# Optimization experiments

Hardware: AMD Instinct MI355X
Metric: run time of the kernel (lower is better)

The kernel has to match this reference:

```python
import jax, jax.numpy as jnp
import numpy as np

KQ = 512
NEG = -1e9


def setup_inputs() -> dict:
    key = jax.random.key(0)
    k1, k2, k3, k4, k5 = jax.random.split(key, 5)
    B, NQ, NK, D, V, O = 16, 1024, 2048, 512, 512, 256
    return {
        "keys": jax.random.normal(k1, (B, NK, D), dtype=jnp.float32),
        "queries": jax.random.normal(k2, (B, NQ, D), dtype=jnp.float32),
        "values": jax.random.normal(k3, (B, NK, V), dtype=jnp.float32),
        "mask": jax.random.randint(k4, (B, NQ, NK), 0, 2, dtype=jnp.int32),
        "W_resize": jax.random.normal(k5, (O, V), dtype=jnp.float32) * (1.0 / np.sqrt(V)),
        "b_resize": jnp.zeros((O,), dtype=jnp.float32),
    }


def reference(keys, queries, values, mask, W_resize, b_resize):
    # score: scaled dot product  [B, NQ, NK]
    logits = jnp.einsum("bqd,bkd->bqk", queries, keys) / jnp.sqrt(jnp.float32(KQ))
    logits = jnp.where(mask == 0, jnp.float32(NEG), logits)
    attn = jax.nn.softmax(logits, axis=-1)
    # context: [B, NQ, V]
    context = jnp.einsum("bqk,bkv->bqv", attn, values)
    # resize to out_size
    context = jnp.einsum("bqv,ov->bqo", context, W_resize) + b_resize
    return context
```

## Files before the change

kernel.cpp:

```cpp
#include <hip/hip_runtime.h>

#define BB   16
#define NQ   1024
#define NK   2048
#define DD   512
#define VV   512
#define OO   256
#define SCALE 0.044194173824159216f

typedef __attribute__((ext_vector_type(4))) float f32x4;
typedef __attribute__((ext_vector_type(8))) short s16x8;

#define AS1(p) ((const __attribute__((address_space(1))) void*)(p))
#define AS3(p) ((__attribute__((address_space(3))) void*)(p))

__device__ __forceinline__ unsigned short f2bf(float f) {
  unsigned u = __float_as_uint(f);
  u += 0x7fffu + ((u >> 16) & 1u);
  return (unsigned short)(u >> 16);
}
__device__ __forceinline__ float bf2f(unsigned short b) {
  return __uint_as_float(((unsigned)b) << 16);
}

__device__ __forceinline__ void gemm_bt_core(
    const unsigned short* __restrict__ Abase,
    const unsigned short* __restrict__ Bbase,
    int K,
    unsigned short* As, unsigned short* Bs,
    f32x4 acc[4][4])
{
  const int t = threadIdx.x;
  const int w = t >> 6;
  const int l = t & 63;
  const int srow = l >> 2;
  const int scol = (l & 3) * 8;
  const int r0 = (w * 2 + 0) * 16 + srow;
  const int r1 = (w * 2 + 1) * 16 + srow;
  const int lds0 = (w * 2 + 0) * 512 + l * 8;
  const int lds1 = (w * 2 + 1) * 512 + l * 8;
  const int wm = (w >> 1) * 64;
  const int wn = (w & 1) * 64;
  const int lm = l & 15;
  const int lq = l >> 4;

  for (int kt = 0; kt < K; kt += 32) {
    __builtin_amdgcn_global_load_lds(AS1(Abase + (size_t)r0 * K + kt + scol), AS3(As + lds0), 16, 0, 0);
    __builtin_amdgcn_global_load_lds(AS1(Abase + (size_t)r1 * K + kt + scol), AS3(As + lds1), 16, 0, 0);
    __builtin_amdgcn_global_load_lds(AS1(Bbase + (size_t)r0 * K + kt + scol), AS3(Bs + lds0), 16, 0, 0);
    __builtin_amdgcn_global_load_lds(AS1(Bbase + (size_t)r1 * K + kt + scol), AS3(Bs + lds1), 16, 0, 0);
    __syncthreads();
    s16x8 af[4], bfr[4];
    #pragma unroll
    for (int i = 0; i < 4; ++i) {
      af[i]  = *(const s16x8*)(As + (wm + i * 16 + lm) * 32 + lq * 8);
      bfr[i] = *(const s16x8*)(Bs + (wn + i * 16 + lm) * 32 + lq * 8);
    }
    #pragma unroll
    for (int mi = 0; mi < 4; ++mi)
      #pragma unroll
      for (int ni = 0; ni < 4; ++ni)
        acc[mi][ni] = __builtin_amdgcn_mfma_f32_16x16x32_bf16(af[mi], bfr[ni], acc[mi][ni], 0, 0, 0);
    __syncthreads();
  }
}


#define CS_STRIDE 136

__global__ __launch_bounds__(256)
void qk_kernel(const unsigned short* __restrict__ Qb,
               const unsigned short* __restrict__ Kb,
               const int* __restrict__ mask,
               unsigned short* __restrict__ S,
               float* __restrict__ sums)
{
  const int b  = blockIdx.z;
  const int tm = blockIdx.y;
  const int tn = blockIdx.x;
  __shared__ unsigned short smem[128 * CS_STRIDE];
  unsigned short* As = smem;
  unsigned short* Bs = smem + 4096;
  unsigned short* Cs = smem;
  const int t = threadIdx.x, w = t >> 6, l = t & 63;
  const int trow = t >> 4, tcol = (t & 15) * 8;

  unsigned mbits0 = 0, mbits1 = 0;
  #pragma unroll
  for (int it = 0; it < 8; ++it) {
    const int row = it * 16 + trow;
    const size_t gbase = ((size_t)b * NQ + tm * 128 + row) * NK + tn * 128 + tcol;
    const int4 m0 = *(const int4*)(mask + gbase);
    const int4 m1 = *(const int4*)(mask + gbase + 4);
    unsigned byte = (m0.x ? 1u : 0u) | (m0.y ? 2u : 0u) | (m0.z ? 4u : 0u) | (m0.w ? 8u : 0u)
                  | (m1.x ? 16u : 0u) | (m1.y ? 32u : 0u) | (m1.z ? 64u : 0u) | (m1.w ? 128u : 0u);
    if (it < 4) mbits0 |= byte << (8 * it);
    else        mbits1 |= byte << (8 * (it - 4));
  }

  f32x4 acc[4][4];
  #pragma unroll
  for (int i = 0; i < 4; ++i)
    #pragma unroll
    for (int j = 0; j < 4; ++j) acc[i][j] = (f32x4){0.f, 0.f, 0.f, 0.f};

  gemm_bt_core(Qb + ((size_t)b * NQ + tm * 128) * DD,
               Kb + ((size_t)b * NK + tn * 128) * DD, DD, As, Bs, acc);

  const int wm = (w >> 1) * 64, wn = (w & 1) * 64;
  const int lm = l & 15, lq = l >> 4;
  #pragma unroll
  for (int mi = 0; mi < 4; ++mi)
    #pragma unroll
    for (int ni = 0; ni < 4; ++ni)
      #pragma unroll
      for (int r = 0; r < 4; ++r)
        Cs[(wm + mi * 16 + lq * 4 + r) * CS_STRIDE + wn + ni * 16 + lm] =
            f2bf(acc[mi][ni][r] * SCALE);
  __syncthreads();

  #pragma unroll
  for (int it = 0; it < 8; ++it) {
    const int row = it * 16 + trow;
    const int gq = tm * 128 + row;
    const size_t gbase = ((size_t)b * NQ + gq) * NK + tn * 128 + tcol;
    s16x8 v = *(const s16x8*)(Cs + row * CS_STRIDE + tcol);
    const unsigned byte = ((it < 4) ? (mbits0 >> (8 * it)) : (mbits1 >> (8 * (it - 4)))) & 0xffu;
    float e[8];
    #pragma unroll
    for (int j = 0; j < 8; ++j)
      e[j] = (byte >> j & 1u) ? __expf(bf2f((unsigned short)v[j])) : 0.f;
    float sp = 0.f;
    #pragma unroll
    for (int j = 0; j < 8; ++j) sp += e[j];
    #pragma unroll
    for (int off = 8; off > 0; off >>= 1) sp += __shfl_down(sp, off, 16);
    if ((t & 15) == 0) atomicAdd(&sums[(size_t)b * NQ + gq], sp);
    s16x8 o;
    #pragma unroll
    for (int j = 0; j < 8; ++j) o[j] = (short)f2bf(e[j]);
    *(s16x8*)(S + gbase) = o;
  }
}

__global__ __launch_bounds__(256)
void pv_kernel(const unsigned short* __restrict__ P,
               const unsigned short* __restrict__ Vt,
               const float* __restrict__ sums,
               unsigned short* __restrict__ Ctx)
{
  const int b  = blockIdx.z;
  const int tm = blockIdx.y;
  const int tn = blockIdx.x;
  __shared__ unsigned short smem[128 * CS_STRIDE];
  __shared__ float Ls[128];
  unsigned short* As = smem;
  unsigned short* Bs = smem + 4096;
  unsigned short* Cs = smem;
  const int t = threadIdx.x;
  if (t < 128) Ls[t] = 1.0f / sums[(size_t)b * NQ + tm * 128 + t];
  f32x4 acc[4][4];
  #pragma unroll
  for (int i = 0; i < 4; ++i)
    #pragma unroll
    for (int j = 0; j < 4; ++j) acc[i][j] = (f32x4){0.f, 0.f, 0.f, 0.f};

  gemm_bt_core(P  + ((size_t)b * NQ + tm * 128) * NK,
               Vt + ((size_t)b * VV + tn * 128) * NK, NK, As, Bs, acc);

  const int w = t >> 6, l = t & 63;
  const int wm = (w >> 1) * 64, wn = (w & 1) * 64;
  const int lm = l & 15, lq = l >> 4;
  #pragma unroll
  for (int mi = 0; mi < 4; ++mi)
    #pragma unroll
    for (int ni = 0; ni < 4; ++ni)
      #pragma unroll
      for (int r = 0; r < 4; ++r) {
        const int row = wm + mi * 16 + lq * 4 + r;
        Cs[row * CS_STRIDE + wn + ni * 16 + lm] = f2bf(acc[mi][ni][r] * Ls[row]);
      }
  __syncthreads();
  const int trow = t >> 4, tcol = (t & 15) * 8;
  #pragma unroll
  for (int it = 0; it < 8; ++it) {
    const int row = it * 16 + trow;
    s16x8 v = *(const s16x8*)(Cs + row * CS_STRIDE + tcol);
    *(s16x8*)(Ctx + ((size_t)b * NQ + tm * 128 + row) * VV + tn * 128 + tcol) = v;
  }
}

#define CSF_STRIDE 136
__global__ __launch_bounds__(256)
void rs_kernel(const unsigned short* __restrict__ Ctx,
               const unsigned short* __restrict__ Wb,
               const float* __restrict__ bias,
               float* __restrict__ out)
{
  const int tm = blockIdx.y;
  const int tn = blockIdx.x;
  __shared__ float smemf[128 * CSF_STRIDE];
  unsigned short* As = (unsigned short*)smemf;
  unsigned short* Bs = (unsigned short*)smemf + 4096;
  float* Cs = smemf;
  f32x4 acc[4][4];
  #pragma unroll
  for (int i = 0; i < 4; ++i)
    #pragma unroll
    for (int j = 0; j < 4; ++j) acc[i][j] = (f32x4){0.f, 0.f, 0.f, 0.f};

  gemm_bt_core(Ctx + (size_t)tm * 128 * VV,
               Wb + (size_t)tn * 128 * VV, VV, As, Bs, acc);

  const int t = threadIdx.x, w = t >> 6, l = t & 63;
  const int wm = (w >> 1) * 64, wn = (w & 1) * 64;
  const int lm = l & 15, lq = l >> 4;
  #pragma unroll
  for (int mi = 0; mi < 4; ++mi)
    #pragma unroll
    for (int ni = 0; ni < 4; ++ni)
      #pragma unroll
      for (int r = 0; r < 4; ++r)
        Cs[(wm + mi * 16 + lq * 4 + r) * CSF_STRIDE + wn + ni * 16 + lm] = acc[mi][ni][r];
  __syncthreads();
  const int trow = t >> 4, tcol = (t & 15) * 8;
  #pragma unroll
  for (int it = 0; it < 8; ++it) {
    const int row = it * 16 + trow;
    f32x4 a = *(const f32x4*)(Cs + row * CSF_STRIDE + tcol);
    f32x4 c = *(const f32x4*)(Cs + row * CSF_STRIDE + tcol + 4);
    const int gn = tn * 128 + tcol;
    const f32x4 b0 = *(const f32x4*)(bias + gn);
    const f32x4 b1 = *(const f32x4*)(bias + gn + 4);
    a += b0; c += b1;
    float* o = out + (size_t)(tm * 128 + row) * OO + gn;
    *(f32x4*)o = a;
    *(f32x4*)(o + 4) = c;
  }
}

#define VT_STRIDE 68
__device__ __forceinline__ void cvt8(const float* __restrict__ in,
                                     unsigned short* __restrict__ out, int i)
{
  const float4* p = (const float4*)in + (size_t)i * 2;
  const float4 a = p[0], b = p[1];
  s16x8 o;
  o[0] = (short)f2bf(a.x); o[1] = (short)f2bf(a.y);
  o[2] = (short)f2bf(a.z); o[3] = (short)f2bf(a.w);
  o[4] = (short)f2bf(b.x); o[5] = (short)f2bf(b.y);
  o[6] = (short)f2bf(b.z); o[7] = (short)f2bf(b.w);
  ((s16x8*)out)[i] = o;
}

__global__ __launch_bounds__(256)
void prep_kernel(const float* __restrict__ q, const float* __restrict__ k,
                 const float* __restrict__ w, const float* __restrict__ v,
                 unsigned short* __restrict__ Qb, unsigned short* __restrict__ Kb,
                 unsigned short* __restrict__ Wb, unsigned short* __restrict__ Vt,
                 float* __restrict__ sums)
{
  __shared__ float tile[64 * VT_STRIDE];
  const int bid = blockIdx.x;
  const int t = threadIdx.x;
  if (bid < 4096) {
    cvt8(q, Qb, bid * 256 + t);
  } else if (bid < 12288) {
    cvt8(k, Kb, (bid - 4096) * 256 + t);
  } else if (bid < 12352) {
    cvt8(w, Wb, (bid - 12288) * 256 + t);
  } else if (bid < 16448) {
    const int flat = bid - 12352;
    const int b  = flat >> 8;
    const int rem = flat & 255;
    const int k0 = (rem >> 3) * 64;
    const int v0 = (rem & 7) * 64;
    const int lr = t >> 4, lc4 = (t & 15) * 4;
    #pragma unroll
    for (int j = 0; j < 4; ++j) {
      const int row = lr + j * 16;
      const float4 x = *(const float4*)(v + ((size_t)b * NK + k0 + row) * VV + v0 + lc4);
      *(float4*)(tile + row * VT_STRIDE + lc4) = x;
    }
    __syncthreads();
    const int vr = t >> 3, kx = (t & 7) * 8;
    #pragma unroll
    for (int j = 0; j < 2; ++j) {
      const int vv = vr + j * 32;
      s16x8 o;
      #pragma unroll
      for (int i = 0; i < 8; ++i) o[i] = (short)f2bf(tile[(kx + i) * VT_STRIDE + vv]);
      *(s16x8*)(Vt + ((size_t)b * VV + v0 + vv) * NK + k0 + kx) = o;
    }
  } else {
    const int i = (bid - 16448) * 256 + t;
    if (i < BB * NQ) sums[i] = 0.f;
  }
}

extern "C" void kernel_launch(void* const* d_in, const int* in_sizes, int n_in,
                              void* d_out, int out_size, void* d_ws, size_t ws_size,
                              hipStream_t stream)
{
  const float* keys    = (const float*)d_in[0];
  const float* queries = (const float*)d_in[1];
  const float* values  = (const float*)d_in[2];
  const int*   mask    = (const int*)  d_in[3];
  const float* W       = (const float*)d_in[4];
  const float* bias    = (const float*)d_in[5];
  float* out = (float*)d_out;

  char* ws = (char*)d_ws;
  unsigned short* Qb = (unsigned short*)(ws);
  unsigned short* Kb = (unsigned short*)(ws + (16ull << 20));
  unsigned short* Vt = (unsigned short*)(ws + (48ull << 20));
  unsigned short* Wb = (unsigned short*)(ws + (80ull << 20));
  unsigned short* S  = (unsigned short*)(ws + (81ull << 20));
  float* sums        = (float*)(ws + (145ull << 20));
  unsigned short* Ctx = Qb;

  prep_kernel<<<dim3(16512), 256, 0, stream>>>(queries, keys, W, values,
                                               Qb, Kb, Wb, Vt, sums);
  qk_kernel<<<dim3(NK / 128, NQ / 128, BB), 256, 0, stream>>>(Qb, Kb, mask, S, sums);
  pv_kernel<<<dim3(VV / 128, NQ / 128, BB), 256, 0, stream>>>(S, Vt, sums, Ctx);
  rs_kernel<<<dim3(OO / 128, (BB * NQ) / 128, 1), 256, 0, stream>>>(Ctx, Wb, bias, out);
}
```

Measured before the change: 465.0 us.

## Fuse QK, masked softmax and PV into a single flash-style kernel

Replaces the separate QK-score kernel (which wrote the bf16 probability matrix to global memory) and the PV kernel with one fused kernel. Each block handles 32 query rows and loops over 128-key tiles, computing scores, masked exponentials and row sums in shared memory, then accumulating P·V in registers. This removes the 64MB intermediate score write and reread and the atomic sum buffer. In exchange the tiles are smaller (32 rows), each block rereads K and V for every 32 queries, and there are many __syncthreads per tile. Like the old code, it skips max-subtraction in the softmax, relying on small logits.

```diff
diff --git a/kernel.cpp b/kernel.cpp
--- a/kernel.cpp
+++ b/kernel.cpp
@@ -21,6 +21,176 @@
 }
 __device__ __forceinline__ float bf2f(unsigned short b) {
   return __uint_as_float(((unsigned)b) << 16);
+}
+
+#define MFMA16(a, b, c) __builtin_amdgcn_mfma_f32_16x16x32_bf16(a, b, c, 0, 0, 0)
+
+__global__ __launch_bounds__(256)
+void flash_kernel(const unsigned short* __restrict__ Qb,
+                  const unsigned short* __restrict__ Kb,
+                  const unsigned short* __restrict__ Vt,
+                  const int* __restrict__ mask,
+                  unsigned short* __restrict__ Ctx)
+{
+  const int b  = blockIdx.y;
+  const int q0 = blockIdx.x * 32;
+  __shared__ unsigned short Qs[32 * 520];
+  __shared__ unsigned short KVs[16640];
+  __shared__ unsigned short Ps[32 * 136];
+  __shared__ float rowsum[32];
+  __shared__ float invs[32];
+
+  const int t = threadIdx.x, w = t >> 6, l = t & 63;
+  const int lm = l & 15, lq = l >> 4;
+  const int sr = l >> 2, sc = (l & 3) * 8;
+
+  f32x4 oacc[2][8];
+  #pragma unroll
+  for (int mi = 0; mi < 2; ++mi)
+    #pragma unroll
+    for (int ni = 0; ni < 8; ++ni) oacc[mi][ni] = (f32x4){0.f, 0.f, 0.f, 0.f};
+
+  #pragma unroll
+  for (int i = 0; i < 8; ++i) {
+    const int row = w * 8 + i;
+    __builtin_amdgcn_global_load_lds(
+        AS1(Qb + ((size_t)(b * NQ + q0 + row)) * DD + l * 8),
+        AS3(Qs + row * 520 + l * 8), 16, 0, 0);
+  }
+  if (t < 32) rowsum[t] = 0.f;
+
+  const int prow = t >> 3, pcol = (t & 7) * 16;
+
+  #pragma unroll 1
+  for (int kt = 0; kt < 16; ++kt) {
+    const size_t mbase = ((size_t)(b * NQ + q0 + prow)) * NK + kt * 128 + pcol;
+    const int4 pm0 = *(const int4*)(mask + mbase);
+    const int4 pm1 = *(const int4*)(mask + mbase + 4);
+    const int4 pm2 = *(const int4*)(mask + mbase + 8);
+    const int4 pm3 = *(const int4*)(mask + mbase + 12);
+
+    f32x4 sacc[2][2];
+    #pragma unroll
+    for (int mi = 0; mi < 2; ++mi)
+      #pragma unroll
+      for (int ni = 0; ni < 2; ++ni) sacc[mi][ni] = (f32x4){0.f, 0.f, 0.f, 0.f};
+
+    const unsigned short* Kbase = Kb + ((size_t)(b * NK + kt * 128)) * DD;
+    #pragma unroll
+    for (int rnd = 0; rnd < 8; ++rnd) {
+      __syncthreads();
+      #pragma unroll
+      for (int c = 0; c < 2; ++c)
+        #pragma unroll
+        for (int i = 0; i < 2; ++i)
+          __builtin_amdgcn_global_load_lds(
+              AS1(Kbase + (size_t)(w * 32 + i * 16 + sr) * DD + rnd * 64 + c * 32 + sc),
+              AS3(KVs + c * 4096 + (w * 32 + i * 16) * 32 + l * 8), 16, 0, 0);
+      __syncthreads();
+      #pragma unroll
+      for (int c = 0; c < 2; ++c) {
+        s16x8 qf[2], kf[2];
+        #pragma unroll
+        for (int mi = 0; mi < 2; ++mi)
+          qf[mi] = *(const s16x8*)(Qs + (mi * 16 + lm) * 520 + rnd * 64 + c * 32 + lq * 8);
+        #pragma unroll
+        for (int ni = 0; ni < 2; ++ni)
+          kf[ni] = *(const s16x8*)(KVs + c * 4096 + (w * 32 + ni * 16 + lm) * 32 + lq * 8);
+        #pragma unroll
+        for (int mi = 0; mi < 2; ++mi)
+          #pragma unroll
+          for (int ni = 0; ni < 2; ++ni)
+            sacc[mi][ni] = MFMA16(qf[mi], kf[ni], sacc[mi][ni]);
+      }
+    }
+
+    #pragma unroll
+    for (int mi = 0; mi < 2; ++mi)
+      #pragma unroll
+      for (int ni = 0; ni < 2; ++ni)
+        #pragma unroll
+        for (int r = 0; r < 4; ++r)
+          Ps[(mi * 16 + lq * 4 + r) * 136 + w * 32 + ni * 16 + lm] =
+              f2bf(sacc[mi][ni][r] * SCALE);
+    __syncthreads();
+
+    {
+      s16x8 p0 = *(const s16x8*)(Ps + prow * 136 + pcol);
+      s16x8 p1 = *(const s16x8*)(Ps + prow * 136 + pcol + 8);
+      float e[16];
+      e[0]  = pm0.x ? __expf(bf2f((unsigned short)p0[0])) : 0.f;
+      e[1]  = pm0.y ? __expf(bf2f((unsigned short)p0[1])) : 0.f;
+      e[2]  = pm0.z ? __expf(bf2f((unsigned short)p0[2])) : 0.f;
+      e[3]  = pm0.w ? __expf(bf2f((unsigned short)p0[3])) : 0.f;
+      e[4]  = pm1.x ? __expf(bf2f((unsigned short)p0[4])) : 0.f;
+      e[5]  = pm1.y ? __expf(bf2f((unsigned short)p0[5])) : 0.f;
+      e[6]  = pm1.z ? __expf(bf2f((unsigned short)p0[6])) : 0.f;
+      e[7]  = pm1.w ? __expf(bf2f((unsigned short)p0[7])) : 0.f;
+      e[8]  = pm2.x ? __expf(bf2f((unsigned short)p1[0])) : 0.f;
+      e[9]  = pm2.y ? __expf(bf2f((unsigned short)p1[1])) : 0.f;
+      e[10] = pm2.z ? __expf(bf2f((unsigned short)p1[2])) : 0.f;
+      e[11] = pm2.w ? __expf(bf2f((unsigned short)p1[3])) : 0.f;
+      e[12] = pm3.x ? __expf(bf2f((unsigned short)p1[4])) : 0.f;
+      e[13] = pm3.y ? __expf(bf2f((unsigned short)p1[5])) : 0.f;
+      e[14] = pm3.z ? __expf(bf2f((unsigned short)p1[6])) : 0.f;
+      e[15] = pm3.w ? __expf(bf2f((unsigned short)p1[7])) : 0.f;
+      float sp = 0.f;
+      s16x8 o0, o1;
+      #pragma unroll
+      for (int j = 0; j < 8; ++j) { o0[j] = (short)f2bf(e[j]); sp += e[j]; }
+      #pragma unroll
+      for (int j = 0; j < 8; ++j) { o1[j] = (short)f2bf(e[8 + j]); sp += e[8 + j]; }
+      *(s16x8*)(Ps + prow * 136 + pcol) = o0;
+      *(s16x8*)(Ps + prow * 136 + pcol + 8) = o1;
+      #pragma unroll
+      for (int off = 4; off > 0; off >>= 1) sp += __shfl_down(sp, off, 8);
+      if ((t & 7) == 0) rowsum[prow] += sp;
+    }
+
+    #pragma unroll
+    for (int cs = 0; cs < 4; ++cs) {
+      __syncthreads();
+      #pragma unroll
+      for (int i = 0; i < 8; ++i)
+        __builtin_amdgcn_global_load_lds(
+            AS1(Vt + ((size_t)(b * VV + w * 128 + i * 16 + sr)) * NK + kt * 128 + cs * 32 + sc),
+            AS3(KVs + (w * 128 + i * 16) * 32 + l * 8), 16, 0, 0);
+      __syncthreads();
+      s16x8 pf[2], vf[8];
+      #pragma unroll
+      for (int mi = 0; mi < 2; ++mi)
+        pf[mi] = *(const s16x8*)(Ps + (mi * 16 + lm) * 136 + cs * 32 + lq * 8);
+      #pragma unroll
+      for (int ni = 0; ni < 8; ++ni)
+        vf[ni] = *(const s16x8*)(KVs + (w * 128 + ni * 16 + lm) * 32 + lq * 8);
+      #pragma unroll
+      for (int mi = 0; mi < 2; ++mi)
+        #pragma unroll
+        for (int ni = 0; ni < 8; ++ni)
+          oacc[mi][ni] = MFMA16(pf[mi], vf[ni], oacc[mi][ni]);
+    }
+  }
+
+  __syncthreads();
+  if (t < 32) invs[t] = 1.f / rowsum[t];
+  __syncthreads();
+  #pragma unroll
+  for (int mi = 0; mi < 2; ++mi)
+    #pragma unroll
+    for (int ni = 0; ni < 8; ++ni)
+      #pragma unroll
+      for (int r = 0; r < 4; ++r) {
+        const int row = mi * 16 + lq * 4 + r;
+        KVs[row * 520 + w * 128 + ni * 16 + lm] = f2bf(oacc[mi][ni][r] * invs[row]);
+      }
+  __syncthreads();
+  const int orow = t >> 3;
+  #pragma unroll
+  for (int it = 0; it < 8; ++it) {
+    const int col = (t & 7) * 8 + it * 64;
+    s16x8 v = *(const s16x8*)(KVs + orow * 520 + col);
+    *(s16x8*)(Ctx + ((size_t)(b * NQ + q0 + orow)) * VV + col) = v;
+  }
 }
 
 __device__ __forceinline__ void gemm_bt_core(
@@ -60,133 +230,8 @@
     for (int mi = 0; mi < 4; ++mi)
       #pragma unroll
       for (int ni = 0; ni < 4; ++ni)
-        acc[mi][ni] = __builtin_amdgcn_mfma_f32_16x16x32_bf16(af[mi], bfr[ni], acc[mi][ni], 0, 0, 0);
+        acc[mi][ni] = MFMA16(af[mi], bfr[ni], acc[mi][ni]);
     __syncthreads();
-  }
-}
-
-
-#define CS_STRIDE 136
-
-__global__ __launch_bounds__(256)
-void qk_kernel(const unsigned short* __restrict__ Qb,
-               const unsigned short* __restrict__ Kb,
-               const int* __restrict__ mask,
-               unsigned short* __restrict__ S,
-               float* __restrict__ sums)
-{
-  const int b  = blockIdx.z;
-  const int tm = blockIdx.y;
-  const int tn = blockIdx.x;
-  __shared__ unsigned short smem[128 * CS_STRIDE];
-  unsigned short* As = smem;
-  unsigned short* Bs = smem + 4096;
-  unsigned short* Cs = smem;
-  const int t = threadIdx.x, w = t >> 6, l = t & 63;
-  const int trow = t >> 4, tcol = (t & 15) * 8;
-
-  unsigned mbits0 = 0, mbits1 = 0;
-  #pragma unroll
-  for (int it = 0; it < 8; ++it) {
-    const int row = it * 16 + trow;
-    const size_t gbase = ((size_t)b * NQ + tm * 128 + row) * NK + tn * 128 + tcol;
-    const int4 m0 = *(const int4*)(mask + gbase);
-    const int4 m1 = *(const int4*)(mask + gbase + 4);
-    unsigned byte = (m0.x ? 1u : 0u) | (m0.y ? 2u : 0u) | (m0.z ? 4u : 0u) | (m0.w ? 8u : 0u)
-                  | (m1.x ? 16u : 0u) | (m1.y ? 32u : 0u) | (m1.z ? 64u : 0u) | (m1.w ? 128u : 0u);
-    if (it < 4) mbits0 |= byte << (8 * it);
-    else        mbits1 |= byte << (8 * (it - 4));
-  }
-
-  f32x4 acc[4][4];
-  #pragma unroll
-  for (int i = 0; i < 4; ++i)
-    #pragma unroll
-    for (int j = 0; j < 4; ++j) acc[i][j] = (f32x4){0.f, 0.f, 0.f, 0.f};
-
-  gemm_bt_core(Qb + ((size_t)b * NQ + tm * 128) * DD,
-               Kb + ((size_t)b * NK + tn * 128) * DD, DD, As, Bs, acc);
-
-  const int wm = (w >> 1) * 64, wn = (w & 1) * 64;
-  const int lm = l & 15, lq = l >> 4;
-  #pragma unroll
-  for (int mi = 0; mi < 4; ++mi)
-    #pragma unroll
-    for (int ni = 0; ni < 4; ++ni)
-      #pragma unroll
-      for (int r = 0; r < 4; ++r)
-        Cs[(wm + mi * 16 + lq * 4 + r) * CS_STRIDE + wn + ni * 16 + lm] =
-            f2bf(acc[mi][ni][r] * SCALE);
-  __syncthreads();
-
-  #pragma unroll
-  for (int it = 0; it < 8; ++it) {
-    const int row = it * 16 + trow;
-    const int gq = tm * 128 + row;
-    const size_t gbase = ((size_t)b * NQ + gq) * NK + tn * 128 + tcol;
-    s16x8 v = *(const s16x8*)(Cs + row * CS_STRIDE + tcol);
-    const unsigned byte = ((it < 4) ? (mbits0 >> (8 * it)) : (mbits1 >> (8 * (it - 4)))) & 0xffu;
-    float e[8];
-    #pragma unroll
-    for (int j = 0; j < 8; ++j)
-      e[j] = (byte >> j & 1u) ? __expf(bf2f((unsigned short)v[j])) : 0.f;
-    float sp = 0.f;
-    #pragma unroll
-    for (int j = 0; j < 8; ++j) sp += e[j];
-    #pragma unroll
-    for (int off = 8; off > 0; off >>= 1) sp += __shfl_down(sp, off, 16);
-    if ((t & 15) == 0) atomicAdd(&sums[(size_t)b * NQ + gq], sp);
-    s16x8 o;
-    #pragma unroll
-    for (int j = 0; j < 8; ++j) o[j] = (short)f2bf(e[j]);
-    *(s16x8*)(S + gbase) = o;
-  }
-}
-
-__global__ __launch_bounds__(256)
-void pv_kernel(const unsigned short* __restrict__ P,
-               const unsigned short* __restrict__ Vt,
-               const float* __restrict__ sums,
-               unsigned short* __restrict__ Ctx)
-{
-  const int b  = blockIdx.z;
-  const int tm = blockIdx.y;
-  const int tn = blockIdx.x;
-  __shared__ unsigned short smem[128 * CS_STRIDE];
-  __shared__ float Ls[128];
-  unsigned short* As = smem;
-  unsigned short* Bs = smem + 4096;
-  unsigned short* Cs = smem;
-  const int t = threadIdx.x;
-  if (t < 128) Ls[t] = 1.0f / sums[(size_t)b * NQ + tm * 128 + t];
-  f32x4 acc[4][4];
-  #pragma unroll
-  for (int i = 0; i < 4; ++i)
-    #pragma unroll
-    for (int j = 0; j < 4; ++j) acc[i][j] = (f32x4){0.f, 0.f, 0.f, 0.f};
-
-  gemm_bt_core(P  + ((size_t)b * NQ + tm * 128) * NK,
-               Vt + ((size_t)b * VV + tn * 128) * NK, NK, As, Bs, acc);
-
-  const int w = t >> 6, l = t & 63;
-  const int wm = (w >> 1) * 64, wn = (w & 1) * 64;
-  const int lm = l & 15, lq = l >> 4;
-  #pragma unroll
-  for (int mi = 0; mi < 4; ++mi)
-    #pragma unroll
-    for (int ni = 0; ni < 4; ++ni)
-      #pragma unroll
-      for (int r = 0; r < 4; ++r) {
-        const int row = wm + mi * 16 + lq * 4 + r;
-        Cs[row * CS_STRIDE + wn + ni * 16 + lm] = f2bf(acc[mi][ni][r] * Ls[row]);
-      }
-  __syncthreads();
-  const int trow = t >> 4, tcol = (t & 15) * 8;
-  #pragma unroll
-  for (int it = 0; it < 8; ++it) {
-    const int row = it * 16 + trow;
-    s16x8 v = *(const s16x8*)(Cs + row * CS_STRIDE + tcol);
-    *(s16x8*)(Ctx + ((size_t)b * NQ + tm * 128 + row) * VV + tn * 128 + tcol) = v;
   }
 }
 
@@ -257,8 +302,7 @@
 void prep_kernel(const float* __restrict__ q, const float* __restrict__ k,
                  const float* __restrict__ w, const float* __restrict__ v,
                  unsigned short* __restrict__ Qb, unsigned short* __restrict__ Kb,
-                 unsigned short* __restrict__ Wb, unsigned short* __restrict__ Vt,
-                 float* __restrict__ sums)
+                 unsigned short* __restrict__ Wb, unsigned short* __restrict__ Vt)
 {
   __shared__ float tile[64 * VT_STRIDE];
   const int bid = blockIdx.x;
@@ -269,7 +313,7 @@
     cvt8(k, Kb, (bid - 4096) * 256 + t);
   } else if (bid < 12352) {
     cvt8(w, Wb, (bid - 12288) * 256 + t);
-  } else if (bid < 16448) {
+  } else {
     const int flat = bid - 12352;
     const int b  = flat >> 8;
     const int rem = flat & 255;
@@ -292,9 +336,6 @@
       for (int i = 0; i < 8; ++i) o[i] = (short)f2bf(tile[(kx + i) * VT_STRIDE + vv]);
       *(s16x8*)(Vt + ((size_t)b * VV + v0 + vv) * NK + k0 + kx) = o;
     }
-  } else {
-    const int i = (bid - 16448) * 256 + t;
-    if (i < BB * NQ) sums[i] = 0.f;
   }
 }
 
@@ -311,17 +352,14 @@
   float* out = (float*)d_out;
 
   char* ws = (char*)d_ws;
-  unsigned short* Qb = (unsigned short*)(ws);
-  unsigned short* Kb = (unsigned short*)(ws + (16ull << 20));
-  unsigned short* Vt = (unsigned short*)(ws + (48ull << 20));
-  unsigned short* Wb = (unsigned short*)(ws + (80ull << 20));
-  unsigned short* S  = (unsigned short*)(ws + (81ull << 20));
-  float* sums        = (float*)(ws + (145ull << 20));
-  unsigned short* Ctx = Qb;
-
-  prep_kernel<<<dim3(16512), 256, 0, stream>>>(queries, keys, W, values,
-                                               Qb, Kb, Wb, Vt, sums);
-  qk_kernel<<<dim3(NK / 128, NQ / 128, BB), 256, 0, stream>>>(Qb, Kb, mask, S, sums);
-  pv_kernel<<<dim3(VV / 128, NQ / 128, BB), 256, 0, stream>>>(S, Vt, sums, Ctx);
+  unsigned short* Qb  = (unsigned short*)(ws);
+  unsigned short* Kb  = (unsigned short*)(ws + (16ull << 20));
+  unsigned short* Vt  = (unsigned short*)(ws + (48ull << 20));
+  unsigned short* Wb  = (unsigned short*)(ws + (80ull << 20));
+  unsigned short* Ctx = (unsigned short*)(ws + (81ull << 20));
+
+  prep_kernel<<<dim3(16448), 256, 0, stream>>>(queries, keys, W, values,
+                                               Qb, Kb, Wb, Vt);
+  flash_kernel<<<dim3(NQ / 32, BB), 256, 0, stream>>>(Qb, Kb, Vt, mask, Ctx);
   rs_kernel<<<dim3(OO / 128, (BB * NQ) / 128, 1), 256, 0, stream>>>(Ctx, Wb, bias, out);
 }
```

New measurement: 499.9 us. 7.5% more time.
